# Kernel optimization log

Measured on AMD Instinct MI355X. Metric: run time of the kernel, lower is better.

Reference implementation:

```python
import jax, jax.numpy as jnp
import numpy as np

# Dimensions: S=Scount nodes, R=Rcount(=n_classes), B=len(source_index)
S, R, IN_F, OUT_F, H, B, C = 10000, 16, 128, 128, 4, 2048, 16
NEG = -9e15


def _bn(x, g, b):
    # BatchNorm1d, training-mode batch statistics (biased var), eps=1e-5
    m = x.mean(0)
    v = x.var(0)
    return (x - m) / jnp.sqrt(v + 1e-5) * g + b


def setup_inputs() -> dict:
    key = jax.random.key(0)
    ks = jax.random.split(key, 13)
    n = lambda k, s: jax.random.normal(k, s, jnp.float32) * 0.1
    return {
        "inter_adj": jax.random.randint(ks[0], (S, R), 0, 2, jnp.int32),
        "city_adj": jax.random.randint(ks[1], (S, S), 0, 2, jnp.int32),
        "province_adj": jax.random.randint(ks[2], (S, S), 0, 2, jnp.int32),
        "source_index": jax.random.randint(ks[3], (B,), 0, S, jnp.int32),
        "Sfeat": n(ks[4], (S, IN_F)),
        "Rfeat": n(ks[5], (R, IN_F)),
        "W1": n(ks[6], (H, IN_F, OUT_F)),
        "W2": n(ks[7], (H, IN_F, OUT_F)),
        "a": n(ks[8], (H, 2 * OUT_F)),
        "a3": n(ks[9], (H, 2 * OUT_F)),
        "a4": n(ks[10], (H, 2 * OUT_F)),
        "bn1_g": jnp.ones((H, OUT_F), jnp.float32),
        "bn1_b": jnp.zeros((H, OUT_F), jnp.float32),
        "bn2_g": jnp.ones((H, OUT_F), jnp.float32),
        "bn2_b": jnp.zeros((H, OUT_F), jnp.float32),
        "outW": n(ks[11], (H * R, C)),
        "outA": n(ks[12], (2 * C,)),
    }


def _forward(inter_adj, city_adj, province_adj, src, Sfeat, Rfeat,
             W1, W2, a, a3, a4, bn1_g, bn1_b, bn2_g, bn2_b, outW, outA):
    Fd = OUT_F
    inter_m = inter_adj > 0            # [S, R]
    city_m = city_adj[src] > 0         # [B, S]
    prov_m = province_adj[src] > 0     # [B, S]
    # Dropout is identity (eval mode); the concat+matmul attention scores are
    # computed as separable rank-1 terms instead of materializing O(S*R*2F).

    def head(W1h, W2h, ah, a3h, a4h, g1h, b1h, g2h, b2h):
        h1 = Rfeat @ W1h               # [R, F]
        h2 = Sfeat @ W2h               # [S, F]
        h2s = h2[src]                  # [B, F]
        # e12[i,j] = lrelu(a[:F].h1[j] + a[F:].h2[i])
        e12 = jax.nn.leaky_relu((h2 @ ah[Fd:])[:, None] + (h1 @ ah[:Fd])[None, :], 0.2)
        att_i = jax.nn.softmax(jnp.where(inter_m, e12, NEG), axis=1)   # [S, R]
        # cat([h3, h3]) -> score constant over the neighbor axis
        e3 = jax.nn.leaky_relu(h2s @ (a3h[:Fd] + a3h[Fd:]), 0.2)[:, None]  # [B,1]
        att3 = jax.nn.softmax(jnp.where(city_m, e3, NEG), axis=1)      # [B, S]
        e4 = jax.nn.leaky_relu(h2s @ (a4h[:Fd] + a4h[Fd:]), 0.2)[:, None]
        att4 = jax.nn.softmax(jnp.where(prov_m, e4, NEG), axis=1)
        InterRC = att_i @ h1                        # [S, F]
        IntraNC = (att3 + att4).T @ h2s             # [S, F]
        v = jax.nn.leaky_relu(_bn(att_i.T @ h2, g1h, b1h), 0.2)  # [R, F]
        u = jax.nn.leaky_relu(_bn(InterRC + IntraNC, g2h, b2h), 0.2)  # [S, F]
        return jax.nn.elu(u @ v.T)                  # [S, R]

    hx = jax.vmap(head)(W1, W2, a, a3, a4, bn1_g, bn1_b, bn2_g, bn2_b)  # [H,S,R]
    x = jnp.transpose(hx, (1, 0, 2)).reshape(S, H * R)
    # output GraphAttentionLayer
    h = x @ outW                                    # [S, C]
    e = jax.nn.leaky_relu(h @ (outA[:C] + outA[C:]), 0.2)[:, None]  # [S,1]
    att = jax.nn.softmax(jnp.where(inter_m, jnp.broadcast_to(e, inter_m.shape), NEG), axis=1)
    # elu inside layer, then elu again in ablation2, then log_softmax
    return jax.nn.log_softmax(jax.nn.elu(jax.nn.elu(att * h)), axis=1)


def reference(inter_adj, city_adj, province_adj, source_index, Sfeat, Rfeat,
              W1, W2, a, a3, a4, bn1_g, bn1_b, bn2_g, bn2_b, outW, outA):
    return _forward(inter_adj, city_adj, province_adj, source_index, Sfeat, Rfeat,
                    W1, W2, a, a3, a4, bn1_g, bn1_b, bn2_g, bn2_b, outW, outA)
```

## Files before the change

kernel.cpp:

```cpp
#include <hip/hip_runtime.h>
#include <hip/hip_bf16.h>
#include <stdint.h>

#define S_N 10000
#define MPAD 10112
#define B_N 2048
#define F_N 128

typedef __bf16 bf16x8 __attribute__((ext_vector_type(8)));
typedef __bf16 bf16x4 __attribute__((ext_vector_type(4)));
typedef float  f32x4  __attribute__((ext_vector_type(4)));
typedef unsigned long long u64;
typedef unsigned int u32;
typedef unsigned short u16;

union Bf8 { u16 us[8]; bf16x8 v; };
union Bh8 { __bf16 h[8]; bf16x8 v; };

__device__ __forceinline__ float lrelu02(float x) { return x >= 0.0f ? x : 0.2f * x; }
__device__ __forceinline__ float eluf(float x)    { return x > 0.0f ? x : expm1f(x); }

__global__ __launch_bounds__(256) void k_bits(const int* __restrict__ adj_c,
        const int* __restrict__ adj_p, const int* __restrict__ src,
        u64* __restrict__ tcity, u64* __restrict__ tprov,
        u32* __restrict__ cc, u32* __restrict__ pc) {
    const int sc = blockIdx.x, wb = blockIdx.y, mat = blockIdx.z;
    const int t = threadIdx.x, l = t & 63, w = t >> 6;
    const int* adj = mat ? adj_p : adj_c;
    u64* tb = mat ? tprov : tcity;
    u32* cnt = mat ? pc : cc;
    __shared__ u64 wt[64][8];
    __shared__ u32 lc[64];
    if (t < 64) lc[t] = 0;
    __syncthreads();
    const int s1 = sc * 512 + t;
    const int s2 = s1 + 256;
    for (int bb = 0; bb < 64; ++bb) {
        int row = src[wb * 64 + bb];
        const int* rp = adj + (size_t)row * S_N;
        int v1 = (s1 < S_N) ? rp[s1] : 0;
        int v2 = (s2 < S_N) ? rp[s2] : 0;
        u64 b1 = __ballot(v1 > 0);
        u64 b2 = __ballot(v2 > 0);
        if (l == 0) {
            wt[bb][w] = b1;
            wt[bb][w + 4] = b2;
            atomicAdd(&lc[bb], (u32)(__popcll(b1) + __popcll(b2)));
        }
    }
    __syncthreads();
    if (t < 64) atomicAdd(&cnt[wb * 64 + t], lc[t]);
    for (int tile = w; tile < 8; tile += 4) {
        u64 wv = wt[l][tile];
        u64 myw = 0;
        #pragma unroll
        for (int j = 0; j < 64; ++j) {
            u64 bal = __ballot((int)((wv >> j) & 1ull));
            if (l == j) myw = bal;
        }
        int s = sc * 512 + tile * 64 + l;
        if (s < MPAD) tb[(size_t)wb * MPAD + s] = myw;
    }
}

__global__ __launch_bounds__(256) void k_prep(const float* __restrict__ Sfeat,
        const int* __restrict__ src, const u32* __restrict__ cc, const u32* __restrict__ pc,
        __bf16* __restrict__ YT, __bf16* __restrict__ ZT, __bf16* __restrict__ SfB) {
    const int bid = blockIdx.x, t = threadIdx.x;
    if (bid < 1024) {
        int idx = bid * 256 + t;
        int f = idx >> 11, b = idx & 2047;
        float sv = Sfeat[src[b] * F_N + f];
        float icc = cc[b] ? 1.0f / (float)cc[b] : 0.0f;
        float ipc = pc[b] ? 1.0f / (float)pc[b] : 0.0f;
        YT[f * B_N + b] = (__bf16)(sv * icc);
        ZT[f * B_N + b] = (__bf16)(sv * ipc);
    } else {
        int i = (bid - 1024) * 256 + t;
        int s = i >> 7;
        SfB[i] = (__bf16)(s < S_N ? Sfeat[i] : 0.0f);
    }
}

__global__ __launch_bounds__(128) void k_small(const float* __restrict__ Rfeat,
        const float* __restrict__ W1, const float* __restrict__ W2, const float* __restrict__ a,
        __bf16* __restrict__ W2T, __bf16* __restrict__ h1T, float* __restrict__ q) {
    __shared__ float red[128];
    int bid = blockIdx.x, t = threadIdx.x;
    if (bid < 64) {
        int h = bid >> 4, r = bid & 15;
        float hv = 0.0f;
        const float* rf = Rfeat + r * F_N;
        const float* wp = W1 + h * F_N * F_N + t;
        for (int k = 0; k < F_N; ++k) hv += rf[k] * wp[k * F_N];
        h1T[(h * F_N + t) * 32 + r] = (__bf16)hv;
        h1T[(h * F_N + t) * 32 + 16 + r] = (__bf16)0.0f;
        red[t] = hv * a[h * 256 + t];
        __syncthreads();
        for (int off = 64; off > 0; off >>= 1) {
            if (t < off) red[t] += red[t + off];
            __syncthreads();
        }
        if (t == 0) q[h * 16 + r] = red[0];
    } else {
        int idx = (bid - 64) * 128 + t;
        int hn = idx >> 7, k = idx & 127;
        int h = hn >> 7, n = hn & 127;
        W2T[idx] = (__bf16)W2[(h * F_N + k) * F_N + n];
    }
}

__global__ __launch_bounds__(256) void g_T(const __bf16* __restrict__ YT, const __bf16* __restrict__ ZT,
        const u64* __restrict__ tcity, const u64* __restrict__ tprov, float* __restrict__ Tp) {
    const int t = threadIdx.x, l = t & 63, w = t >> 6;
    const int wm = w >> 1, wn = w & 1;
    const int quad = l >> 4, ln = l & 15;
    const int s_blk = blockIdx.x * 128;
    const unsigned char* cb = (const unsigned char*)tcity;
    const unsigned char* pb = (const unsigned char*)tprov;
    const f32x4 fz = {0.0f, 0.0f, 0.0f, 0.0f};
    f32x4 acc[4][4];
    #pragma unroll
    for (int mt = 0; mt < 4; ++mt)
        #pragma unroll
        for (int nt = 0; nt < 4; ++nt) acc[mt][nt] = fz;
    const int k_base = blockIdx.y * 512;
    for (int it = 0; it < 16; ++it) {
        int kk = k_base + it * 32;
        bf16x8 Ya[4], Za[4];
        #pragma unroll
        for (int mt = 0; mt < 4; ++mt) {
            int f = wm * 64 + mt * 16 + ln;
            Ya[mt] = *(const bf16x8*)(YT + f * B_N + kk + quad * 8);
            Za[mt] = *(const bf16x8*)(ZT + f * B_N + kk + quad * 8);
        }
        bf16x8 Bc[4], Bp[4];
        #pragma unroll
        for (int nt = 0; nt < 4; ++nt) {
            int s = s_blk + wn * 64 + nt * 16 + ln;
            size_t base = ((size_t)(kk >> 6) * MPAD + s) * 8 + ((kk >> 3) & 7) + quad;
            unsigned int cby = cb[base], pby = pb[base];
            Bf8 uc, up;
            #pragma unroll
            for (int j = 0; j < 8; ++j) {
                uc.us[j] = ((cby >> j) & 1u) ? (u16)0x3F80 : (u16)0;
                up.us[j] = ((pby >> j) & 1u) ? (u16)0x3F80 : (u16)0;
            }
            Bc[nt] = uc.v; Bp[nt] = up.v;
        }
        #pragma unroll
        for (int mt = 0; mt < 4; ++mt)
            #pragma unroll
            for (int nt = 0; nt < 4; ++nt) {
                acc[mt][nt] = __builtin_amdgcn_mfma_f32_16x16x32_bf16(Ya[mt], Bc[nt], acc[mt][nt], 0, 0, 0);
                acc[mt][nt] = __builtin_amdgcn_mfma_f32_16x16x32_bf16(Za[mt], Bp[nt], acc[mt][nt], 0, 0, 0);
            }
    }
    float* tp = Tp + (size_t)blockIdx.y * ((size_t)MPAD * F_N);
    #pragma unroll
    for (int nt = 0; nt < 4; ++nt) {
        int s = s_blk + wn * 64 + nt * 16 + ln;
        #pragma unroll
        for (int mt = 0; mt < 4; ++mt) {
            int f0 = wm * 64 + mt * 16 + quad * 4;
            *(f32x4*)(tp + (size_t)s * F_N + f0) = acc[mt][nt];
        }
    }
}

__global__ __launch_bounds__(256) void k_tred(const float* __restrict__ Tp, __bf16* __restrict__ Tb) {
    int i4 = blockIdx.x * 256 + threadIdx.x;
    size_t base = (size_t)i4 * 4;
    const size_t stride = (size_t)MPAD * F_N;
    f32x4 s0 = *(const f32x4*)(Tp + base);
    f32x4 s1 = *(const f32x4*)(Tp + stride + base);
    f32x4 s2 = *(const f32x4*)(Tp + 2 * stride + base);
    f32x4 s3 = *(const f32x4*)(Tp + 3 * stride + base);
    f32x4 sum = s0 + s1 + s2 + s3;
    bf16x4 o;
    #pragma unroll
    for (int j = 0; j < 4; ++j) o[j] = (__bf16)sum[j];
    *(bf16x4*)(Tb + base) = o;
}

__global__ __launch_bounds__(256) void g_h2att(const __bf16* __restrict__ A, const __bf16* __restrict__ W2T,
        const float* __restrict__ a, const float* __restrict__ q, const int* __restrict__ inter,
        __bf16* __restrict__ h2b, float* __restrict__ att, __bf16* __restrict__ attb) {
    const int t = threadIdx.x, l = t & 63, w = t >> 6;
    const int wm = w >> 1, wn = w & 1, quad = l >> 4, ln = l & 15;
    const int s0 = blockIdx.x * 128, h = blockIdx.y;
    const f32x4 fz = {0.0f, 0.0f, 0.0f, 0.0f};
    f32x4 acc[4][4];
    #pragma unroll
    for (int mt = 0; mt < 4; ++mt)
        #pragma unroll
        for (int nt = 0; nt < 4; ++nt) acc[mt][nt] = fz;
    #pragma unroll
    for (int it = 0; it < 4; ++it) {
        int kk = it * 32;
        bf16x8 af[4], bfr[4];
        #pragma unroll
        for (int mt = 0; mt < 4; ++mt)
            af[mt] = *(const bf16x8*)(A + (size_t)(s0 + wm * 64 + mt * 16 + ln) * F_N + kk + quad * 8);
        #pragma unroll
        for (int nt = 0; nt < 4; ++nt)
            bfr[nt] = *(const bf16x8*)(W2T + (size_t)(h * F_N + wn * 64 + nt * 16 + ln) * F_N + kk + quad * 8);
        #pragma unroll
        for (int mt = 0; mt < 4; ++mt)
            #pragma unroll
            for (int nt = 0; nt < 4; ++nt)
                acc[mt][nt] = __builtin_amdgcn_mfma_f32_16x16x32_bf16(af[mt], bfr[nt], acc[mt][nt], 0, 0, 0);
    }
    __shared__ float ps[128];
    if (t < 128) ps[t] = 0.0f;
    __syncthreads();
    float a2v[4];
    #pragma unroll
    for (int nt = 0; nt < 4; ++nt) a2v[nt] = a[h * 256 + 128 + wn * 64 + nt * 16 + ln];
    #pragma unroll
    for (int mt = 0; mt < 4; ++mt) {
        #pragma unroll
        for (int r = 0; r < 4; ++r) {
            int s = s0 + wm * 64 + mt * 16 + quad * 4 + r;
            float pp = 0.0f;
            #pragma unroll
            for (int nt = 0; nt < 4; ++nt) {
                float val = acc[mt][nt][r];
                h2b[((size_t)h * MPAD + s) * F_N + wn * 64 + nt * 16 + ln] = (__bf16)val;
                pp += val * a2v[nt];
            }
            #pragma unroll
            for (int m = 8; m > 0; m >>= 1) pp += __shfl_xor(pp, m, 16);
            if (ln == 0) atomicAdd(&ps[wm * 64 + mt * 16 + quad * 4 + r], pp);
        }
    }
    __syncthreads();
    if (t < 128) {
        int s = s0 + t;
        if (s < S_N) {
            float pv = ps[t];
            float e[16];
            int msk[16], cn = 0;
            float mx = -3e38f;
            #pragma unroll
            for (int c = 0; c < 16; ++c) {
                msk[c] = inter[s * 16 + c] > 0;
                cn += msk[c];
                e[c] = lrelu02(pv + q[h * 16 + c]);
                if (msk[c]) mx = fmaxf(mx, e[c]);
            }
            float sm = 0.0f;
            #pragma unroll
            for (int c = 0; c < 16; ++c) {
                e[c] = msk[c] ? expf(e[c] - mx) : 0.0f;
                sm += e[c];
            }
            float inv = cn > 0 ? 1.0f / sm : 0.0f;
            #pragma unroll
            for (int c = 0; c < 16; ++c) {
                float av = cn > 0 ? e[c] * inv : 0.0625f;
                att[((size_t)h * MPAD + s) * 16 + c] = av;
                attb[((size_t)h * MPAD + s) * 16 + c] = (__bf16)av;
            }
        } else {
            #pragma unroll
            for (int c = 0; c < 16; ++c) {
                att[((size_t)h * MPAD + s) * 16 + c] = 0.0f;
                attb[((size_t)h * MPAD + s) * 16 + c] = (__bf16)0.0f;
            }
        }
    }
}

__global__ __launch_bounds__(256) void g_P(const __bf16* __restrict__ Tb, const __bf16* __restrict__ W2T,
        const __bf16* __restrict__ attb, const __bf16* __restrict__ h1T,
        float* __restrict__ P, float* __restrict__ usum, float* __restrict__ usq) {
    const int t = threadIdx.x, l = t & 63, w = t >> 6;
    const int wm = w >> 1, wn = w & 1, quad = l >> 4, ln = l & 15;
    const int s0 = blockIdx.x * 128, h = blockIdx.y;
    const f32x4 fz = {0.0f, 0.0f, 0.0f, 0.0f};
    f32x4 acc[4][4];
    #pragma unroll
    for (int mt = 0; mt < 4; ++mt)
        #pragma unroll
        for (int nt = 0; nt < 4; ++nt) acc[mt][nt] = fz;
    {
        bf16x8 a2[4], b2[4];
        #pragma unroll
        for (int mt = 0; mt < 4; ++mt) {
            int s = s0 + wm * 64 + mt * 16 + ln;
            Bf8 az;
            az.v = *(const bf16x8*)(attb + ((size_t)h * MPAD + s) * 16 + (quad & 1) * 8);
            if (quad >= 2) {
                #pragma unroll
                for (int j = 0; j < 8; ++j) az.us[j] = 0;
            }
            a2[mt] = az.v;
        }
        #pragma unroll
        for (int nt = 0; nt < 4; ++nt) {
            int f = wn * 64 + nt * 16 + ln;
            b2[nt] = *(const bf16x8*)(h1T + ((size_t)(h * F_N + f)) * 32 + quad * 8);
        }
        #pragma unroll
        for (int mt = 0; mt < 4; ++mt)
            #pragma unroll
            for (int nt = 0; nt < 4; ++nt)
                acc[mt][nt] = __builtin_amdgcn_mfma_f32_16x16x32_bf16(a2[mt], b2[nt], acc[mt][nt], 0, 0, 0);
    }
    #pragma unroll
    for (int it = 0; it < 4; ++it) {
        int kk = it * 32;
        bf16x8 af[4], bfr[4];
        #pragma unroll
        for (int mt = 0; mt < 4; ++mt)
            af[mt] = *(const bf16x8*)(Tb + (size_t)(s0 + wm * 64 + mt * 16 + ln) * F_N + kk + quad * 8);
        #pragma unroll
        for (int nt = 0; nt < 4; ++nt)
            bfr[nt] = *(const bf16x8*)(W2T + (size_t)(h * F_N + wn * 64 + nt * 16 + ln) * F_N + kk + quad * 8);
        #pragma unroll
        for (int mt = 0; mt < 4; ++mt)
            #pragma unroll
            for (int nt = 0; nt < 4; ++nt)
                acc[mt][nt] = __builtin_amdgcn_mfma_f32_16x16x32_bf16(af[mt], bfr[nt], acc[mt][nt], 0, 0, 0);
    }
    __shared__ float lsum[128], lsq[128];
    if (t < 128) { lsum[t] = 0.0f; lsq[t] = 0.0f; }
    __syncthreads();
    #pragma unroll
    for (int nt = 0; nt < 4; ++nt) {
        int f = wn * 64 + nt * 16 + ln;
        float p1 = 0.0f, p2 = 0.0f;
        #pragma unroll
        for (int mt = 0; mt < 4; ++mt) {
            int sb = s0 + wm * 64 + mt * 16 + quad * 4;
            #pragma unroll
            for (int r = 0; r < 4; ++r) {
                float val = acc[mt][nt][r];
                P[((size_t)h * MPAD + sb + r) * F_N + f] = val;
                p1 += val; p2 += val * val;
            }
        }
        atomicAdd(&lsum[f], p1);
        atomicAdd(&lsq[f], p2);
    }
    __syncthreads();
    if (t < 128) {
        atomicAdd(&usum[h * F_N + t], lsum[t]);
        atomicAdd(&usq[h * F_N + t], lsq[t]);
    }
}

__global__ __launch_bounds__(128) void k_M(const float* __restrict__ att, const __bf16* __restrict__ h2b,
        float* __restrict__ M) {
    const int h = blockIdx.y, t = threadIdx.x;
    const int s0 = blockIdx.x * 200;
    float acc[16] = {};
    for (int s = s0; s < s0 + 200; ++s) {
        float hv = (float)h2b[((size_t)h * MPAD + s) * F_N + t];
        const float* ar = att + ((size_t)h * MPAD + s) * 16;
        #pragma unroll
        for (int r = 0; r < 16; ++r) acc[r] += ar[r] * hv;
    }
    #pragma unroll
    for (int r = 0; r < 16; ++r) atomicAdd(&M[(h * 16 + r) * F_N + t], acc[r]);
}

__global__ __launch_bounds__(128) void k_bn(const float* __restrict__ usum, const float* __restrict__ usq,
        const float* __restrict__ M, const float* __restrict__ g1, const float* __restrict__ b1,
        const float* __restrict__ g2, const float* __restrict__ b2,
        float* __restrict__ scale_u, float* __restrict__ shift_u, __bf16* __restrict__ vb) {
    const int h = blockIdx.x, f = threadIdx.x;
    const int i = h * F_N + f;
    float mean = usum[i] * (1.0f / S_N);
    float var = usq[i] * (1.0f / S_N) - mean * mean;
    float sc = g2[i] * rsqrtf(var + 1e-5f);
    scale_u[i] = sc;
    shift_u[i] = b2[i] - mean * sc;
    float mv[16], s1 = 0.0f, s2 = 0.0f;
    #pragma unroll
    for (int r = 0; r < 16; ++r) {
        mv[r] = M[(h * 16 + r) * F_N + f];
        s1 += mv[r]; s2 += mv[r] * mv[r];
    }
    float m1 = s1 * 0.0625f, v1 = s2 * 0.0625f - m1 * m1;
    float g = g1[i] * rsqrtf(v1 + 1e-5f);
    float bb = b1[i] - m1 * g;
    #pragma unroll
    for (int r = 0; r < 16; ++r)
        vb[(h * 16 + r) * F_N + f] = (__bf16)lrelu02(mv[r] * g + bb);
}

__global__ __launch_bounds__(128) void g_G(const float* __restrict__ P, const float* __restrict__ scale_u,
        const float* __restrict__ shift_u, const __bf16* __restrict__ vb, float* __restrict__ G) {
    const int t = threadIdx.x, l = t & 63, w = t >> 6;
    const int quad = l >> 4, ln = l & 15;
    const int s0 = blockIdx.x * 128, h = blockIdx.y;
    __shared__ float scl[128], shl[128];
    scl[t] = scale_u[h * F_N + t];
    shl[t] = shift_u[h * F_N + t];
    __syncthreads();
    const f32x4 fz = {0.0f, 0.0f, 0.0f, 0.0f};
    f32x4 acc[4] = {fz, fz, fz, fz};
    #pragma unroll
    for (int it = 0; it < 4; ++it) {
        int kk = it * 32;
        bf16x8 bfr = *(const bf16x8*)(vb + ((size_t)(h * 16 + ln)) * F_N + kk + quad * 8);
        #pragma unroll
        for (int mt = 0; mt < 4; ++mt) {
            int s = s0 + w * 64 + mt * 16 + ln;
            const float* pp = P + ((size_t)h * MPAD + s) * F_N + kk + quad * 8;
            f32x4 p0 = *(const f32x4*)pp;
            f32x4 p1 = *(const f32x4*)(pp + 4);
            Bh8 af;
            #pragma unroll
            for (int j = 0; j < 4; ++j) {
                int f = kk + quad * 8 + j;
                af.h[j]     = (__bf16)lrelu02(p0[j] * scl[f]     + shl[f]);
                af.h[j + 4] = (__bf16)lrelu02(p1[j] * scl[f + 4] + shl[f + 4]);
            }
            acc[mt] = __builtin_amdgcn_mfma_f32_16x16x32_bf16(af.v, bfr, acc[mt], 0, 0, 0);
        }
    }
    #pragma unroll
    for (int mt = 0; mt < 4; ++mt)
        #pragma unroll
        for (int r = 0; r < 4; ++r) {
            int s = s0 + w * 64 + mt * 16 + quad * 4 + r;
            G[(size_t)s * 64 + h * 16 + ln] = eluf(acc[mt][r]);
        }
}

__global__ __launch_bounds__(256) void k_fin(const float* __restrict__ G, const float* __restrict__ outW,
        const int* __restrict__ inter, float* __restrict__ out) {
    const int t = threadIdx.x;
    const int s0 = blockIdx.x * 16;
    __shared__ float Wl[64 * 16];
    __shared__ float Gl[16 * 64];
    #pragma unroll
    for (int k = 0; k < 4; ++k) {
        int i = k * 256 + t;
        Wl[i] = outW[i];
        Gl[i] = G[(size_t)(s0 + (i >> 6)) * 64 + (i & 63)];
    }
    __syncthreads();
    const int ss = t >> 4, c = t & 15, s = s0 + ss;
    float hm = 0.0f;
    #pragma unroll
    for (int j = 0; j < 64; ++j) hm += Gl[ss * 64 + j] * Wl[j * 16 + c];
    int msk = inter[s * 16 + c] > 0;
    int cn = msk;
    #pragma unroll
    for (int m = 8; m > 0; m >>= 1) cn += __shfl_xor(cn, m, 16);
    float attf = cn > 0 ? (msk ? 1.0f / (float)cn : 0.0f) : 0.0625f;
    float y = eluf(eluf(attf * hm));
    float mx = y;
    #pragma unroll
    for (int m = 8; m > 0; m >>= 1) mx = fmaxf(mx, __shfl_xor(mx, m, 16));
    float ex = expf(y - mx);
    float sm = ex;
    #pragma unroll
    for (int m = 8; m > 0; m >>= 1) sm += __shfl_xor(sm, m, 16);
    out[s * 16 + c] = y - mx - logf(sm);
}

extern "C" void kernel_launch(void* const* d_in, const int* in_sizes, int n_in,
                              void* d_out, int out_size, void* d_ws, size_t ws_size,
                              hipStream_t stream) {
    const int* inter = (const int*)d_in[0];
    const int* city  = (const int*)d_in[1];
    const int* prov  = (const int*)d_in[2];
    const int* src   = (const int*)d_in[3];
    const float* Sfeat = (const float*)d_in[4];
    const float* Rfeat = (const float*)d_in[5];
    const float* W1 = (const float*)d_in[6];
    const float* W2 = (const float*)d_in[7];
    const float* a  = (const float*)d_in[8];
    const float* g1 = (const float*)d_in[11];
    const float* b1 = (const float*)d_in[12];
    const float* g2 = (const float*)d_in[13];
    const float* b2 = (const float*)d_in[14];
    const float* outW = (const float*)d_in[15];
    float* out = (float*)d_out;

    char* p = (char*)d_ws;
    float* M    = (float*)p; p += 4 * 16 * F_N * 4;
    float* usum = (float*)p; p += 2048;
    float* usq  = (float*)p; p += 2048;
    u32*   cc   = (u32*)p;   p += 8192;
    u32*   pc   = (u32*)p;   p += 8192;
    size_t zbytes = (size_t)(p - (char*)d_ws);
    u64* tcity = (u64*)p; p += 32 * (size_t)MPAD * 8;
    u64* tprov = (u64*)p; p += 32 * (size_t)MPAD * 8;
    __bf16* YT  = (__bf16*)p; p += (size_t)F_N * B_N * 2;
    __bf16* ZT  = (__bf16*)p; p += (size_t)F_N * B_N * 2;
    __bf16* SfB = (__bf16*)p; p += (size_t)MPAD * F_N * 2;
    __bf16* W2T = (__bf16*)p; p += 512 * 128 * 2;
    __bf16* h1T = (__bf16*)p; p += 4 * 128 * 32 * 2;
    float*  q   = (float*)p;  p += 512;
    float*  Tp  = (float*)p;  p += 4 * (size_t)MPAD * F_N * 4;
    __bf16* Tb  = (__bf16*)p; p += (size_t)MPAD * F_N * 2;
    __bf16* h2b = (__bf16*)p; p += 4 * (size_t)MPAD * F_N * 2;
    float*  att = (float*)p;  p += 4 * (size_t)MPAD * 16 * 4;
    __bf16* attb= (__bf16*)p; p += 4 * (size_t)MPAD * 16 * 2;
    float*  P   = (float*)p;  p += 4 * (size_t)MPAD * F_N * 4;
    float* scale_u = (float*)p; p += 2048;
    float* shift_u = (float*)p; p += 2048;
    __bf16* vb  = (__bf16*)p; p += 4 * 16 * 128 * 2;
    float*  G   = (float*)p;  p += (size_t)MPAD * 64 * 4;

    hipMemsetAsync(d_ws, 0, zbytes, stream);
    k_bits <<<dim3(20, 32, 2), 256, 0, stream>>>(city, prov, src, tcity, tprov, cc, pc);
    k_prep <<<6080, 256, 0, stream>>>(Sfeat, src, cc, pc, YT, ZT, SfB);
    k_small<<<576, 128, 0, stream>>>(Rfeat, W1, W2, a, W2T, h1T, q);
    g_T    <<<dim3(79, 4), 256, 0, stream>>>(YT, ZT, tcity, tprov, Tp);
    k_tred <<<1264, 256, 0, stream>>>(Tp, Tb);
    g_h2att<<<dim3(79, 4), 256, 0, stream>>>(SfB, W2T, a, q, inter, h2b, att, attb);
    g_P    <<<dim3(79, 4), 256, 0, stream>>>(Tb, W2T, attb, h1T, P, usum, usq);
    k_M    <<<dim3(50, 4), 128, 0, stream>>>(att, h2b, M);
    k_bn   <<<4, 128, 0, stream>>>(usum, usq, M, g1, b1, g2, b2, scale_u, shift_u, vb);
    g_G    <<<dim3(79, 4), 128, 0, stream>>>(P, scale_u, shift_u, vb, G);
    k_fin  <<<625, 256, 0, stream>>>(G, outW, inter, out);
}
```

Measured before the change: 861.9 us.

## Fuse prep kernels, fold M reduction into h2 GEMM, merge BN/G/final stages

Merges the bit-packing, Sfeat conversion, W2 transpose and h1/q computations into a single launch, and splits the YT/ZT scaling into its own kernel. The h2 GEMM now keeps h2 and the attention weights in shared memory and computes the att^T·h2 product with MFMA plus global atomics, so the h2b and fp32 att buffers and the separate k_M pass are gone. The BN statistics, v computation, G GEMM and final output layer are fused into one kernel. This cuts launch count and intermediate global traffic, at the cost of redundant per-block BN/v recomputation and more atomic contention on M.

Measured after the change: 791.1 us. 8.2% less time.

```diff
diff --git a/kernel.cpp b/kernel.cpp
--- a/kernel.cpp
+++ b/kernel.cpp
@@ -20,94 +20,96 @@
 __device__ __forceinline__ float lrelu02(float x) { return x >= 0.0f ? x : 0.2f * x; }
 __device__ __forceinline__ float eluf(float x)    { return x > 0.0f ? x : expm1f(x); }
 
-__global__ __launch_bounds__(256) void k_bits(const int* __restrict__ adj_c,
+__global__ __launch_bounds__(256) void k_bits_pre(const int* __restrict__ adj_c,
         const int* __restrict__ adj_p, const int* __restrict__ src,
+        const float* __restrict__ Sfeat, const float* __restrict__ Rfeat,
+        const float* __restrict__ W1, const float* __restrict__ W2, const float* __restrict__ a,
         u64* __restrict__ tcity, u64* __restrict__ tprov,
-        u32* __restrict__ cc, u32* __restrict__ pc) {
-    const int sc = blockIdx.x, wb = blockIdx.y, mat = blockIdx.z;
-    const int t = threadIdx.x, l = t & 63, w = t >> 6;
-    const int* adj = mat ? adj_p : adj_c;
-    u64* tb = mat ? tprov : tcity;
-    u32* cnt = mat ? pc : cc;
-    __shared__ u64 wt[64][8];
-    __shared__ u32 lc[64];
-    if (t < 64) lc[t] = 0;
-    __syncthreads();
-    const int s1 = sc * 512 + t;
-    const int s2 = s1 + 256;
-    for (int bb = 0; bb < 64; ++bb) {
-        int row = src[wb * 64 + bb];
-        const int* rp = adj + (size_t)row * S_N;
-        int v1 = (s1 < S_N) ? rp[s1] : 0;
-        int v2 = (s2 < S_N) ? rp[s2] : 0;
-        u64 b1 = __ballot(v1 > 0);
-        u64 b2 = __ballot(v2 > 0);
-        if (l == 0) {
-            wt[bb][w] = b1;
-            wt[bb][w + 4] = b2;
-            atomicAdd(&lc[bb], (u32)(__popcll(b1) + __popcll(b2)));
-        }
-    }
-    __syncthreads();
-    if (t < 64) atomicAdd(&cnt[wb * 64 + t], lc[t]);
-    for (int tile = w; tile < 8; tile += 4) {
-        u64 wv = wt[l][tile];
-        u64 myw = 0;
-        #pragma unroll
-        for (int j = 0; j < 64; ++j) {
-            u64 bal = __ballot((int)((wv >> j) & 1ull));
-            if (l == j) myw = bal;
-        }
-        int s = sc * 512 + tile * 64 + l;
-        if (s < MPAD) tb[(size_t)wb * MPAD + s] = myw;
-    }
-}
-
-__global__ __launch_bounds__(256) void k_prep(const float* __restrict__ Sfeat,
-        const int* __restrict__ src, const u32* __restrict__ cc, const u32* __restrict__ pc,
-        __bf16* __restrict__ YT, __bf16* __restrict__ ZT, __bf16* __restrict__ SfB) {
+        u32* __restrict__ cc, u32* __restrict__ pc,
+        __bf16* __restrict__ SfB, __bf16* __restrict__ W2T, __bf16* __restrict__ h1T,
+        float* __restrict__ q) {
     const int bid = blockIdx.x, t = threadIdx.x;
-    if (bid < 1024) {
-        int idx = bid * 256 + t;
-        int f = idx >> 11, b = idx & 2047;
-        float sv = Sfeat[src[b] * F_N + f];
-        float icc = cc[b] ? 1.0f / (float)cc[b] : 0.0f;
-        float ipc = pc[b] ? 1.0f / (float)pc[b] : 0.0f;
-        YT[f * B_N + b] = (__bf16)(sv * icc);
-        ZT[f * B_N + b] = (__bf16)(sv * ipc);
-    } else {
-        int i = (bid - 1024) * 256 + t;
+    if (bid < 1280) {
+        const int sc = bid % 20, wb = (bid / 20) % 32, mat = bid / 640;
+        const int l = t & 63, w = t >> 6;
+        const int* adj = mat ? adj_p : adj_c;
+        u64* tb = mat ? tprov : tcity;
+        u32* cnt = mat ? pc : cc;
+        __shared__ u64 wt[64][8];
+        __shared__ u32 lc[64];
+        if (t < 64) lc[t] = 0;
+        __syncthreads();
+        const int s1 = sc * 512 + t;
+        const int s2 = s1 + 256;
+        for (int bb = 0; bb < 64; ++bb) {
+            int row = src[wb * 64 + bb];
+            const int* rp = adj + (size_t)row * S_N;
+            int v1 = (s1 < S_N) ? rp[s1] : 0;
+            int v2 = (s2 < S_N) ? rp[s2] : 0;
+            u64 b1 = __ballot(v1 > 0);
+            u64 b2 = __ballot(v2 > 0);
+            if (l == 0) {
+                wt[bb][w] = b1;
+                wt[bb][w + 4] = b2;
+                atomicAdd(&lc[bb], (u32)(__popcll(b1) + __popcll(b2)));
+            }
+        }
+        __syncthreads();
+        if (t < 64) atomicAdd(&cnt[wb * 64 + t], lc[t]);
+        for (int tile = w; tile < 8; tile += 4) {
+            u64 wv = wt[l][tile];
+            u64 myw = 0;
+            #pragma unroll
+            for (int j = 0; j < 64; ++j) {
+                u64 bal = __ballot((int)((wv >> j) & 1ull));
+                if (l == j) myw = bal;
+            }
+            int s = sc * 512 + tile * 64 + l;
+            if (s < MPAD) tb[(size_t)wb * MPAD + s] = myw;
+        }
+    } else if (bid < 6336) {
+        int i = (bid - 1280) * 256 + t;
         int s = i >> 7;
         SfB[i] = (__bf16)(s < S_N ? Sfeat[i] : 0.0f);
-    }
-}
-
-__global__ __launch_bounds__(128) void k_small(const float* __restrict__ Rfeat,
-        const float* __restrict__ W1, const float* __restrict__ W2, const float* __restrict__ a,
-        __bf16* __restrict__ W2T, __bf16* __restrict__ h1T, float* __restrict__ q) {
-    __shared__ float red[128];
-    int bid = blockIdx.x, t = threadIdx.x;
-    if (bid < 64) {
-        int h = bid >> 4, r = bid & 15;
-        float hv = 0.0f;
-        const float* rf = Rfeat + r * F_N;
-        const float* wp = W1 + h * F_N * F_N + t;
-        for (int k = 0; k < F_N; ++k) hv += rf[k] * wp[k * F_N];
-        h1T[(h * F_N + t) * 32 + r] = (__bf16)hv;
-        h1T[(h * F_N + t) * 32 + 16 + r] = (__bf16)0.0f;
-        red[t] = hv * a[h * 256 + t];
-        __syncthreads();
-        for (int off = 64; off > 0; off >>= 1) {
-            if (t < off) red[t] += red[t + off];
-            __syncthreads();
-        }
-        if (t == 0) q[h * 16 + r] = red[0];
-    } else {
-        int idx = (bid - 64) * 128 + t;
+    } else if (bid < 6592) {
+        int idx = (bid - 6336) * 256 + t;
         int hn = idx >> 7, k = idx & 127;
         int h = hn >> 7, n = hn & 127;
         W2T[idx] = (__bf16)W2[(h * F_N + k) * F_N + n];
-    }
+    } else {
+        __shared__ float red[256];
+        int b2i = bid - 6592;
+        int h = b2i >> 4, r = b2i & 15;
+        float hv = 0.0f;
+        if (t < 128) {
+            const float* rf = Rfeat + r * F_N;
+            const float* wp = W1 + h * F_N * F_N + t;
+            for (int k = 0; k < F_N; ++k) hv += rf[k] * wp[k * F_N];
+        }
+        red[t] = (t < 128) ? hv * a[h * 256 + t] : 0.0f;
+        __syncthreads();
+        for (int off = 128; off > 0; off >>= 1) {
+            if (t < off) red[t] += red[t + off];
+            __syncthreads();
+        }
+        if (t == 0) q[h * 16 + r] = red[0];
+        if (t < 128) {
+            h1T[(h * F_N + t) * 32 + r] = (__bf16)hv;
+            h1T[(h * F_N + t) * 32 + 16 + r] = (__bf16)0.0f;
+        }
+    }
+}
+
+__global__ __launch_bounds__(256) void k_yz(const float* __restrict__ Sfeat,
+        const int* __restrict__ src, const u32* __restrict__ cc, const u32* __restrict__ pc,
+        __bf16* __restrict__ YT, __bf16* __restrict__ ZT) {
+    int idx = blockIdx.x * 256 + threadIdx.x;
+    int f = idx >> 11, b = idx & 2047;
+    float sv = Sfeat[src[b] * F_N + f];
+    float icc = cc[b] ? 1.0f / (float)cc[b] : 0.0f;
+    float ipc = pc[b] ? 1.0f / (float)pc[b] : 0.0f;
+    YT[f * B_N + b] = (__bf16)(sv * icc);
+    ZT[f * B_N + b] = (__bf16)(sv * ipc);
 }
 
 __global__ __launch_bounds__(256) void g_T(const __bf16* __restrict__ YT, const __bf16* __restrict__ ZT,
@@ -183,12 +185,17 @@
     *(bf16x4*)(Tb + base) = o;
 }
 
-__global__ __launch_bounds__(256) void g_h2att(const __bf16* __restrict__ A, const __bf16* __restrict__ W2T,
+__global__ __launch_bounds__(256) void g_h2attM(const __bf16* __restrict__ A, const __bf16* __restrict__ W2T,
         const float* __restrict__ a, const float* __restrict__ q, const int* __restrict__ inter,
-        __bf16* __restrict__ h2b, float* __restrict__ att, __bf16* __restrict__ attb) {
+        __bf16* __restrict__ attb, float* __restrict__ Mg) {
     const int t = threadIdx.x, l = t & 63, w = t >> 6;
     const int wm = w >> 1, wn = w & 1, quad = l >> 4, ln = l & 15;
     const int s0 = blockIdx.x * 128, h = blockIdx.y;
+    __shared__ __bf16 h2T[128 * 136];
+    __shared__ __bf16 attT[16 * 136];
+    __shared__ float ps[128];
+    if (t < 128) ps[t] = 0.0f;
+    __syncthreads();
     const f32x4 fz = {0.0f, 0.0f, 0.0f, 0.0f};
     f32x4 acc[4][4];
     #pragma unroll
@@ -211,24 +218,23 @@
             for (int nt = 0; nt < 4; ++nt)
                 acc[mt][nt] = __builtin_amdgcn_mfma_f32_16x16x32_bf16(af[mt], bfr[nt], acc[mt][nt], 0, 0, 0);
     }
-    __shared__ float ps[128];
-    if (t < 128) ps[t] = 0.0f;
-    __syncthreads();
     float a2v[4];
     #pragma unroll
     for (int nt = 0; nt < 4; ++nt) a2v[nt] = a[h * 256 + 128 + wn * 64 + nt * 16 + ln];
     #pragma unroll
     for (int mt = 0; mt < 4; ++mt) {
         #pragma unroll
+        for (int nt = 0; nt < 4; ++nt) {
+            bf16x4 o;
+            #pragma unroll
+            for (int j = 0; j < 4; ++j) o[j] = (__bf16)acc[mt][nt][j];
+            *(bf16x4*)(&h2T[(wn * 64 + nt * 16 + ln) * 136 + wm * 64 + mt * 16 + quad * 4]) = o;
+        }
+        #pragma unroll
         for (int r = 0; r < 4; ++r) {
-            int s = s0 + wm * 64 + mt * 16 + quad * 4 + r;
             float pp = 0.0f;
             #pragma unroll
-            for (int nt = 0; nt < 4; ++nt) {
-                float val = acc[mt][nt][r];
-                h2b[((size_t)h * MPAD + s) * F_N + wn * 64 + nt * 16 + ln] = (__bf16)val;
-                pp += val * a2v[nt];
-            }
+            for (int nt = 0; nt < 4; ++nt) pp += acc[mt][nt][r] * a2v[nt];
             #pragma unroll
             for (int m = 8; m > 0; m >>= 1) pp += __shfl_xor(pp, m, 16);
             if (ln == 0) atomicAdd(&ps[wm * 64 + mt * 16 + quad * 4 + r], pp);
@@ -259,16 +265,31 @@
             #pragma unroll
             for (int c = 0; c < 16; ++c) {
                 float av = cn > 0 ? e[c] * inv : 0.0625f;
-                att[((size_t)h * MPAD + s) * 16 + c] = av;
                 attb[((size_t)h * MPAD + s) * 16 + c] = (__bf16)av;
+                attT[c * 136 + t] = (__bf16)av;
             }
         } else {
             #pragma unroll
             for (int c = 0; c < 16; ++c) {
-                att[((size_t)h * MPAD + s) * 16 + c] = 0.0f;
                 attb[((size_t)h * MPAD + s) * 16 + c] = (__bf16)0.0f;
-            }
-        }
+                attT[c * 136 + t] = (__bf16)0.0f;
+            }
+        }
+    }
+    __syncthreads();
+    #pragma unroll
+    for (int fi = 0; fi < 2; ++fi) {
+        int ft = 2 * w + fi;
+        f32x4 macc = fz;
+        #pragma unroll
+        for (int kit = 0; kit < 4; ++kit) {
+            bf16x8 av = *(const bf16x8*)(&attT[ln * 136 + kit * 32 + quad * 8]);
+            bf16x8 bv = *(const bf16x8*)(&h2T[(ft * 16 + ln) * 136 + kit * 32 + quad * 8]);
+            macc = __builtin_amdgcn_mfma_f32_16x16x32_bf16(av, bv, macc, 0, 0, 0);
+        }
+        #pragma unroll
+        for (int r = 0; r < 4; ++r)
+            atomicAdd(&Mg[(h * 16 + quad * 4 + r) * F_N + ft * 16 + ln], macc[r]);
     }
 }
 
@@ -351,117 +372,104 @@
     }
 }
 
-__global__ __launch_bounds__(128) void k_M(const float* __restrict__ att, const __bf16* __restrict__ h2b,
-        float* __restrict__ M) {
-    const int h = blockIdx.y, t = threadIdx.x;
-    const int s0 = blockIdx.x * 200;
-    float acc[16] = {};
-    for (int s = s0; s < s0 + 200; ++s) {
-        float hv = (float)h2b[((size_t)h * MPAD + s) * F_N + t];
-        const float* ar = att + ((size_t)h * MPAD + s) * 16;
-        #pragma unroll
-        for (int r = 0; r < 16; ++r) acc[r] += ar[r] * hv;
-    }
-    #pragma unroll
-    for (int r = 0; r < 16; ++r) atomicAdd(&M[(h * 16 + r) * F_N + t], acc[r]);
-}
-
-__global__ __launch_bounds__(128) void k_bn(const float* __restrict__ usum, const float* __restrict__ usq,
-        const float* __restrict__ M, const float* __restrict__ g1, const float* __restrict__ b1,
+__global__ __launch_bounds__(256) void g_out(const float* __restrict__ P,
+        const float* __restrict__ usum, const float* __restrict__ usq, const float* __restrict__ Mg,
+        const float* __restrict__ g1, const float* __restrict__ b1,
         const float* __restrict__ g2, const float* __restrict__ b2,
-        float* __restrict__ scale_u, float* __restrict__ shift_u, __bf16* __restrict__ vb) {
-    const int h = blockIdx.x, f = threadIdx.x;
-    const int i = h * F_N + f;
-    float mean = usum[i] * (1.0f / S_N);
-    float var = usq[i] * (1.0f / S_N) - mean * mean;
-    float sc = g2[i] * rsqrtf(var + 1e-5f);
-    scale_u[i] = sc;
-    shift_u[i] = b2[i] - mean * sc;
-    float mv[16], s1 = 0.0f, s2 = 0.0f;
-    #pragma unroll
-    for (int r = 0; r < 16; ++r) {
-        mv[r] = M[(h * 16 + r) * F_N + f];
-        s1 += mv[r]; s2 += mv[r] * mv[r];
-    }
-    float m1 = s1 * 0.0625f, v1 = s2 * 0.0625f - m1 * m1;
-    float g = g1[i] * rsqrtf(v1 + 1e-5f);
-    float bb = b1[i] - m1 * g;
-    #pragma unroll
-    for (int r = 0; r < 16; ++r)
-        vb[(h * 16 + r) * F_N + f] = (__bf16)lrelu02(mv[r] * g + bb);
-}
-
-__global__ __launch_bounds__(128) void g_G(const float* __restrict__ P, const float* __restrict__ scale_u,
-        const float* __restrict__ shift_u, const __bf16* __restrict__ vb, float* __restrict__ G) {
-    const int t = threadIdx.x, l = t & 63, w = t >> 6;
-    const int quad = l >> 4, ln = l & 15;
-    const int s0 = blockIdx.x * 128, h = blockIdx.y;
-    __shared__ float scl[128], shl[128];
-    scl[t] = scale_u[h * F_N + t];
-    shl[t] = shift_u[h * F_N + t];
-    __syncthreads();
+        const float* __restrict__ outW, const int* __restrict__ inter, float* __restrict__ out) {
+    const int t = threadIdx.x, l = t & 63, w = t >> 6, quad = l >> 4, ln = l & 15;
+    const int s0 = blockIdx.x * 64;
+    __shared__ __bf16 v_lds[64 * 136];
+    __shared__ float G_lds[64 * 68];
+    __shared__ float scs[512], shs[512];
+    __shared__ float W_lds[1024];
+    for (int i = t; i < 1024; i += 256) W_lds[i] = outW[i];
+    if (t < 128) {
+        #pragma unroll
+        for (int h = 0; h < 4; ++h) {
+            int i = h * F_N + t;
+            float mean = usum[i] * (1.0f / S_N);
+            float var = usq[i] * (1.0f / S_N) - mean * mean;
+            float sc = g2[i] * rsqrtf(var + 1e-5f);
+            scs[i] = sc;
+            shs[i] = b2[i] - mean * sc;
+        }
+    }
+    {
+        int f = t & 127;
+        int hb = (t >> 7) * 2;
+        #pragma unroll
+        for (int hh = hb; hh < hb + 2; ++hh) {
+            float mv[16], s1 = 0.0f, s2 = 0.0f;
+            #pragma unroll
+            for (int r = 0; r < 16; ++r) {
+                mv[r] = Mg[(hh * 16 + r) * F_N + f];
+                s1 += mv[r]; s2 += mv[r] * mv[r];
+            }
+            float m1 = s1 * 0.0625f, v1 = s2 * 0.0625f - m1 * m1;
+            int i = hh * F_N + f;
+            float g = g1[i] * rsqrtf(v1 + 1e-5f);
+            float bb = b1[i] - m1 * g;
+            #pragma unroll
+            for (int r = 0; r < 16; ++r)
+                v_lds[(hh * 16 + r) * 136 + f] = (__bf16)lrelu02(mv[r] * g + bb);
+        }
+    }
+    __syncthreads();
+    const int h = w;
     const f32x4 fz = {0.0f, 0.0f, 0.0f, 0.0f};
-    f32x4 acc[4] = {fz, fz, fz, fz};
-    #pragma unroll
-    for (int it = 0; it < 4; ++it) {
-        int kk = it * 32;
-        bf16x8 bfr = *(const bf16x8*)(vb + ((size_t)(h * 16 + ln)) * F_N + kk + quad * 8);
-        #pragma unroll
-        for (int mt = 0; mt < 4; ++mt) {
-            int s = s0 + w * 64 + mt * 16 + ln;
-            const float* pp = P + ((size_t)h * MPAD + s) * F_N + kk + quad * 8;
+    #pragma unroll
+    for (int mt = 0; mt < 4; ++mt) {
+        f32x4 gacc = fz;
+        int s = s0 + mt * 16 + ln;
+        #pragma unroll
+        for (int kit = 0; kit < 4; ++kit) {
+            int k0 = kit * 32 + quad * 8;
+            const float* pp = P + ((size_t)h * MPAD + s) * F_N + k0;
             f32x4 p0 = *(const f32x4*)pp;
             f32x4 p1 = *(const f32x4*)(pp + 4);
+            f32x4 c0 = *(const f32x4*)(scs + h * F_N + k0);
+            f32x4 c1 = *(const f32x4*)(scs + h * F_N + k0 + 4);
+            f32x4 d0 = *(const f32x4*)(shs + h * F_N + k0);
+            f32x4 d1 = *(const f32x4*)(shs + h * F_N + k0 + 4);
             Bh8 af;
             #pragma unroll
             for (int j = 0; j < 4; ++j) {
-                int f = kk + quad * 8 + j;
-                af.h[j]     = (__bf16)lrelu02(p0[j] * scl[f]     + shl[f]);
-                af.h[j + 4] = (__bf16)lrelu02(p1[j] * scl[f + 4] + shl[f + 4]);
-            }
-            acc[mt] = __builtin_amdgcn_mfma_f32_16x16x32_bf16(af.v, bfr, acc[mt], 0, 0, 0);
-        }
-    }
-    #pragma unroll
-    for (int mt = 0; mt < 4; ++mt)
-        #pragma unroll
-        for (int r = 0; r < 4; ++r) {
-            int s = s0 + w * 64 + mt * 16 + quad * 4 + r;
-            G[(size_t)s * 64 + h * 16 + ln] = eluf(acc[mt][r]);
-        }
-}
-
-__global__ __launch_bounds__(256) void k_fin(const float* __restrict__ G, const float* __restrict__ outW,
-        const int* __restrict__ inter, float* __restrict__ out) {
-    const int t = threadIdx.x;
-    const int s0 = blockIdx.x * 16;
-    __shared__ float Wl[64 * 16];
-    __shared__ float Gl[16 * 64];
-    #pragma unroll
-    for (int k = 0; k < 4; ++k) {
-        int i = k * 256 + t;
-        Wl[i] = outW[i];
-        Gl[i] = G[(size_t)(s0 + (i >> 6)) * 64 + (i & 63)];
-    }
-    __syncthreads();
-    const int ss = t >> 4, c = t & 15, s = s0 + ss;
-    float hm = 0.0f;
-    #pragma unroll
-    for (int j = 0; j < 64; ++j) hm += Gl[ss * 64 + j] * Wl[j * 16 + c];
-    int msk = inter[s * 16 + c] > 0;
-    int cn = msk;
-    #pragma unroll
-    for (int m = 8; m > 0; m >>= 1) cn += __shfl_xor(cn, m, 16);
-    float attf = cn > 0 ? (msk ? 1.0f / (float)cn : 0.0f) : 0.0625f;
-    float y = eluf(eluf(attf * hm));
-    float mx = y;
-    #pragma unroll
-    for (int m = 8; m > 0; m >>= 1) mx = fmaxf(mx, __shfl_xor(mx, m, 16));
-    float ex = expf(y - mx);
-    float sm = ex;
-    #pragma unroll
-    for (int m = 8; m > 0; m >>= 1) sm += __shfl_xor(sm, m, 16);
-    out[s * 16 + c] = y - mx - logf(sm);
+                af.h[j]     = (__bf16)lrelu02(p0[j] * c0[j] + d0[j]);
+                af.h[j + 4] = (__bf16)lrelu02(p1[j] * c1[j] + d1[j]);
+            }
+            bf16x8 bv = *(const bf16x8*)(&v_lds[(h * 16 + ln) * 136 + k0]);
+            gacc = __builtin_amdgcn_mfma_f32_16x16x32_bf16(af.v, bv, gacc, 0, 0, 0);
+        }
+        #pragma unroll
+        for (int r = 0; r < 4; ++r)
+            G_lds[(mt * 16 + quad * 4 + r) * 68 + h * 16 + ln] = eluf(gacc[r]);
+    }
+    __syncthreads();
+    const int c = t & 15, ss = t >> 4;
+    #pragma unroll
+    for (int pass = 0; pass < 4; ++pass) {
+        int sl = pass * 16 + ss;
+        int s = s0 + sl;
+        float hm = 0.0f;
+        #pragma unroll
+        for (int j = 0; j < 64; ++j) hm += G_lds[sl * 68 + j] * W_lds[j * 16 + c];
+        int valid = s < S_N;
+        int msk = valid ? (inter[(valid ? s : 0) * 16 + c] > 0) : 0;
+        int cn = msk;
+        #pragma unroll
+        for (int m = 8; m > 0; m >>= 1) cn += __shfl_xor(cn, m, 16);
+        float attf = cn > 0 ? (msk ? 1.0f / (float)cn : 0.0f) : 0.0625f;
+        float y = eluf(eluf(attf * hm));
+        float mx = y;
+        #pragma unroll
+        for (int m = 8; m > 0; m >>= 1) mx = fmaxf(mx, __shfl_xor(mx, m, 16));
+        float ex = expf(y - mx);
+        float sm = ex;
+        #pragma unroll
+        for (int m = 8; m > 0; m >>= 1) sm += __shfl_xor(sm, m, 16);
+        if (valid) out[s * 16 + c] = y - mx - logf(sm);
+    }
 }
 
 extern "C" void kernel_launch(void* const* d_in, const int* in_sizes, int n_in,
@@ -500,25 +508,16 @@
     float*  q   = (float*)p;  p += 512;
     float*  Tp  = (float*)p;  p += 4 * (size_t)MPAD * F_N * 4;
     __bf16* Tb  = (__bf16*)p; p += (size_t)MPAD * F_N * 2;
-    __bf16* h2b = (__bf16*)p; p += 4 * (size_t)MPAD * F_N * 2;
-    float*  att = (float*)p;  p += 4 * (size_t)MPAD * 16 * 4;
     __bf16* attb= (__bf16*)p; p += 4 * (size_t)MPAD * 16 * 2;
     float*  P   = (float*)p;  p += 4 * (size_t)MPAD * F_N * 4;
-    float* scale_u = (float*)p; p += 2048;
-    float* shift_u = (float*)p; p += 2048;
-    __bf16* vb  = (__bf16*)p; p += 4 * 16 * 128 * 2;
-    float*  G   = (float*)p;  p += (size_t)MPAD * 64 * 4;
 
     hipMemsetAsync(d_ws, 0, zbytes, stream);
-    k_bits <<<dim3(20, 32, 2), 256, 0, stream>>>(city, prov, src, tcity, tprov, cc, pc);
-    k_prep <<<6080, 256, 0, stream>>>(Sfeat, src, cc, pc, YT, ZT, SfB);
-    k_small<<<576, 128, 0, stream>>>(Rfeat, W1, W2, a, W2T, h1T, q);
-    g_T    <<<dim3(79, 4), 256, 0, stream>>>(YT, ZT, tcity, tprov, Tp);
-    k_tred <<<1264, 256, 0, stream>>>(Tp, Tb);
-    g_h2att<<<dim3(79, 4), 256, 0, stream>>>(SfB, W2T, a, q, inter, h2b, att, attb);
-    g_P    <<<dim3(79, 4), 256, 0, stream>>>(Tb, W2T, attb, h1T, P, usum, usq);
-    k_M    <<<dim3(50, 4), 128, 0, stream>>>(att, h2b, M);
-    k_bn   <<<4, 128, 0, stream>>>(usum, usq, M, g1, b1, g2, b2, scale_u, shift_u, vb);
-    g_G    <<<dim3(79, 4), 128, 0, stream>>>(P, scale_u, shift_u, vb, G);
-    k_fin  <<<625, 256, 0, stream>>>(G, outW, inter, out);
-}
+    k_bits_pre<<<6656, 256, 0, stream>>>(city, prov, src, Sfeat, Rfeat, W1, W2, a,
+                                         tcity, tprov, cc, pc, SfB, W2T, h1T, q);
+    k_yz      <<<1024, 256, 0, stream>>>(Sfeat, src, cc, pc, YT, ZT);
+    g_T       <<<dim3(79, 4), 256, 0, stream>>>(YT, ZT, tcity, tprov, Tp);
+    k_tred    <<<1264, 256, 0, stream>>>(Tp, Tb);
+    g_h2attM  <<<dim3(79, 4), 256, 0, stream>>>(SfB, W2T, a, q, inter, attb, M);
+    g_P       <<<dim3(79, 4), 256, 0, stream>>>(Tb, W2T, attb, h1T, P, usum, usq);
+    g_out     <<<157, 256, 0, stream>>>(P, usum, usq, M, g1, b1, g2, b2, outW, inter, out);
+}
```
